# Kernel optimization log

Measured on AMD Instinct MI355X. Metric: run time of the kernel, lower is better.

Reference implementation:

```python
import jax, jax.numpy as jnp
import numpy as np

ALPHA = 0.1


def setup_inputs() -> dict:
    key = jax.random.key(0)
    k1, k2, k3, k4 = jax.random.split(key, 4)
    B, S, D = 64, 2048, 512
    n_mask, n_unmask = 1536, 512
    return {
        "outputs": jax.random.normal(k1, (B, S, D), dtype=jnp.float32),
        "orig_image": jax.random.normal(k2, (B, S, D), dtype=jnp.float32),
        "mask_id": jax.random.randint(k3, (B, n_mask), 0, S, dtype=jnp.int64),
        "unmask_id": jax.random.randint(k4, (B, n_unmask), 0, S, dtype=jnp.int64),
    }


def _per_sample_mse(outputs, orig, idx):
    # gather [B, n_idx, D] rows, then MSE (mean reduction) per sample -> [B]
    pred = jnp.take_along_axis(outputs, idx[:, :, None], axis=1)
    tgt = jnp.take_along_axis(orig, idx[:, :, None], axis=1)
    return jnp.mean((pred - tgt) ** 2, axis=(1, 2))


def reference(outputs, orig_image, mask_id, unmask_id):
    # sum_i loss_i / b  ==  mean over batch of per-sample MSE
    masked = _per_sample_mse(outputs, orig_image, mask_id)    # [B]
    unmasked = _per_sample_mse(outputs, orig_image, unmask_id)  # [B]
    return jnp.mean(masked) + ALPHA * jnp.mean(unmasked)
```

## Files before the change

### kernel.cpp

```cpp
#include <hip/hip_runtime.h>
#include <hip/hip_bf16.h>

constexpr int B_DIM   = 64;
constexpr int S_DIM   = 2048;
constexpr int D_DIM   = 512;
constexpr int NMASK   = 1536;
constexpr int NUNMASK = 512;
constexpr float ALPHA = 0.1f;

constexpr int ROWS_PER_SAMPLE = NMASK + NUNMASK;
constexpr int ROWS_TOTAL      = B_DIM * ROWS_PER_SAMPLE;
constexpr int BLOCK           = 256;
constexpr int GRID            = 2048;

__global__ __launch_bounds__(BLOCK) void mae_loss_kernel(
    const float* __restrict__ outputs,
    const float* __restrict__ orig,
    const int*   __restrict__ mask_id,
    const int*   __restrict__ unmask_id,
    float*       __restrict__ out)
{
    const int lane_in_row  = threadIdx.x & 127;
    const int row_in_block = threadIdx.x >> 7;

    const float wm = 1.0f / (float)((long long)B_DIM * NMASK   * D_DIM);
    const float wu = ALPHA / (float)((long long)B_DIM * NUNMASK * D_DIM);

    float acc = 0.0f;

    for (int r = blockIdx.x * 2 + row_in_block; r < ROWS_TOTAL; r += GRID * 2) {
        const int b = r >> 11;
        const int j = r & 2047;
        int   idx;
        float w;
        if (j < NMASK) {
            idx = mask_id[b * NMASK + j];
            w   = wm;
        } else {
            idx = unmask_id[b * NUNMASK + (j - NMASK)];
            w   = wu;
        }
        const size_t row_off = ((size_t)b * S_DIM + (size_t)idx) * D_DIM;
        const float4* po = (const float4*)(outputs + row_off);
        const float4* pt = (const float4*)(orig    + row_off);
        const float4 o = po[lane_in_row];
        const float4 t = pt[lane_in_row];
        const float dx = o.x - t.x;
        const float dy = o.y - t.y;
        const float dz = o.z - t.z;
        const float dw = o.w - t.w;
        acc += w * (dx * dx + dy * dy + dz * dz + dw * dw);
    }

    #pragma unroll
    for (int off = 32; off > 0; off >>= 1)
        acc += __shfl_down(acc, off, 64);

    __shared__ float sdata[BLOCK / 64];
    const int wid = threadIdx.x >> 6;
    if ((threadIdx.x & 63) == 0) sdata[wid] = acc;
    __syncthreads();

    if (threadIdx.x == 0) {
        float s = 0.0f;
        #pragma unroll
        for (int i = 0; i < BLOCK / 64; ++i) s += sdata[i];
        atomicAdd(out, s);
    }
}

extern "C" void kernel_launch(void* const* d_in, const int* in_sizes, int n_in,
                              void* d_out, int out_size, void* d_ws, size_t ws_size,
                              hipStream_t stream) {
    const float* outputs   = (const float*)d_in[0];
    const float* orig      = (const float*)d_in[1];
    const int*   mask_id   = (const int*)d_in[2];
    const int*   unmask_id = (const int*)d_in[3];
    float* out = (float*)d_out;

    hipMemsetAsync(out, 0, sizeof(float), stream);

    mae_loss_kernel<<<GRID, BLOCK, 0, stream>>>(outputs, orig, mask_id, unmask_id, out);
}
```

Measured before the change: 490.7 us.

## Replace row gather with per-row weight histogram and a streaming weighted SSE

```diff
diff --git a/kernel.cpp b/kernel.cpp
--- a/kernel.cpp
+++ b/kernel.cpp
@@ -8,48 +8,60 @@
 constexpr int NUNMASK = 512;
 constexpr float ALPHA = 0.1f;
 
-constexpr int ROWS_PER_SAMPLE = NMASK + NUNMASK;
-constexpr int ROWS_TOTAL      = B_DIM * ROWS_PER_SAMPLE;
-constexpr int BLOCK           = 256;
-constexpr int GRID            = 2048;
+constexpr int N_MASK_TOT   = B_DIM * NMASK;
+constexpr int N_UNMASK_TOT = B_DIM * NUNMASK;
+constexpr int N_IDX_TOT    = N_MASK_TOT + N_UNMASK_TOT;
+constexpr int ROWS_TOTAL   = B_DIM * S_DIM;
 
-__global__ __launch_bounds__(BLOCK) void mae_loss_kernel(
+constexpr int BLOCK = 256;
+constexpr int GRID  = 2048;
+
+__global__ __launch_bounds__(256) void build_weights_kernel(
+    const int* __restrict__ mask_id,
+    const int* __restrict__ unmask_id,
+    float*     __restrict__ w)
+{
+    const int tid = blockIdx.x * 256 + threadIdx.x;
+    if (tid >= N_IDX_TOT) return;
+
+    const float wm = 1.0f / (float)((long long)B_DIM * NMASK   * D_DIM);
+    const float wu = ALPHA / (float)((long long)B_DIM * NUNMASK * D_DIM);
+
+    if (tid < N_MASK_TOT) {
+        const int b   = tid / NMASK;
+        const int idx = mask_id[tid];
+        atomicAdd(w + b * S_DIM + idx, wm);
+    } else {
+        const int u   = tid - N_MASK_TOT;
+        const int b   = u / NUNMASK;
+        const int idx = unmask_id[u];
+        atomicAdd(w + b * S_DIM + idx, wu);
+    }
+}
+
+__global__ __launch_bounds__(BLOCK) void weighted_sse_kernel(
     const float* __restrict__ outputs,
     const float* __restrict__ orig,
-    const int*   __restrict__ mask_id,
-    const int*   __restrict__ unmask_id,
+    const float* __restrict__ wrow,
     float*       __restrict__ out)
 {
     const int lane_in_row  = threadIdx.x & 127;
     const int row_in_block = threadIdx.x >> 7;
 
-    const float wm = 1.0f / (float)((long long)B_DIM * NMASK   * D_DIM);
-    const float wu = ALPHA / (float)((long long)B_DIM * NUNMASK * D_DIM);
-
     float acc = 0.0f;
 
     for (int r = blockIdx.x * 2 + row_in_block; r < ROWS_TOTAL; r += GRID * 2) {
-        const int b = r >> 11;
-        const int j = r & 2047;
-        int   idx;
-        float w;
-        if (j < NMASK) {
-            idx = mask_id[b * NMASK + j];
-            w   = wm;
-        } else {
-            idx = unmask_id[b * NUNMASK + (j - NMASK)];
-            w   = wu;
+        const float w = wrow[r];
+        if (w != 0.0f) {
+            const size_t row_off = (size_t)r * D_DIM;
+            const float4 o = ((const float4*)(outputs + row_off))[lane_in_row];
+            const float4 t = ((const float4*)(orig    + row_off))[lane_in_row];
+            const float dx = o.x - t.x;
+            const float dy = o.y - t.y;
+            const float dz = o.z - t.z;
+            const float dw = o.w - t.w;
+            acc += w * (dx * dx + dy * dy + dz * dz + dw * dw);
         }
-        const size_t row_off = ((size_t)b * S_DIM + (size_t)idx) * D_DIM;
-        const float4* po = (const float4*)(outputs + row_off);
-        const float4* pt = (const float4*)(orig    + row_off);
-        const float4 o = po[lane_in_row];
-        const float4 t = pt[lane_in_row];
-        const float dx = o.x - t.x;
-        const float dy = o.y - t.y;
-        const float dz = o.z - t.z;
-        const float dw = o.w - t.w;
-        acc += w * (dx * dx + dy * dy + dz * dz + dw * dw);
     }
 
     #pragma unroll
@@ -76,9 +88,14 @@
     const float* orig      = (const float*)d_in[1];
     const int*   mask_id   = (const int*)d_in[2];
     const int*   unmask_id = (const int*)d_in[3];
-    float* out = (float*)d_out;
+    float* out  = (float*)d_out;
+    float* wrow = (float*)d_ws;
 
-    hipMemsetAsync(out, 0, sizeof(float), stream);
+    hipMemsetAsync(out,  0, sizeof(float), stream);
+    hipMemsetAsync(wrow, 0, (size_t)ROWS_TOTAL * sizeof(float), stream);
 
-    mae_loss_kernel<<<GRID, BLOCK, 0, stream>>>(outputs, orig, mask_id, unmask_id, out);
+    build_weights_kernel<<<(N_IDX_TOT + 255) / 256, 256, 0, stream>>>(
+        mask_id, unmask_id, wrow);
+
+    weighted_sse_kernel<<<GRID, BLOCK, 0, stream>>>(outputs, orig, wrow, out);
 }
```

After: 494.7 us. About the same (+0.8%).
